# Performance work log

Measured on AMD Instinct MI355X. Metric: run time of the kernel, lower is better.

Reference implementation:

```python
import jax, jax.numpy as jnp
import numpy as np

EMB = 768
HEADS = 12
DH = EMB // HEADS


def setup_inputs() -> dict:
    key = jax.random.key(0)
    k = jax.random.split(key, 5)
    s = 0.02
    return {
        "x": jax.random.normal(k[0], (4, 2048, EMB), dtype=jnp.float32),
        "qkv_w": jax.random.normal(k[1], (3 * EMB, EMB), dtype=jnp.float32) * s,  # torch Linear weight [out,in]
        "qkv_b": jax.random.normal(k[2], (3 * EMB,), dtype=jnp.float32) * s,
        "proj_w": jax.random.normal(k[3], (EMB, EMB), dtype=jnp.float32) * s,
        "proj_b": jax.random.normal(k[4], (EMB,), dtype=jnp.float32) * s,
    }


def reference(x, qkv_w, qkv_b, proj_w, proj_b):
    b, n, _ = x.shape
    qkv = x @ qkv_w.T + qkv_b  # [b, n, 3*EMB]
    # rearrange 'b n (h d qkv) -> qkv b h n d'
    qkv = qkv.reshape(b, n, HEADS, DH, 3)
    qkv = jnp.transpose(qkv, (4, 0, 2, 1, 3))  # [3, b, h, n, d]
    q, k, v = qkv[0], qkv[1], qkv[2]
    e = jnp.einsum("bhqd,bhkd->bhqk", q, k)
    scale = jnp.float32(EMB) ** 0.5
    # NOTE: original divides by sqrt(emb_size) AFTER softmax (faithful to source)
    attn = jax.nn.softmax(e, axis=-1) / scale
    out = jnp.einsum("bhqk,bhkd->bhqd", attn, v)
    out = jnp.transpose(out, (0, 2, 1, 3)).reshape(b, n, EMB)  # 'b h n d -> b n (h d)'
    return out @ proj_w.T + proj_b
```

## Files before the change

kernel.cpp:

```cpp
#include <hip/hip_runtime.h>
#include <hip/hip_bf16.h>

typedef unsigned short ushort_t;
typedef __attribute__((ext_vector_type(8))) short s16x8;
typedef __attribute__((ext_vector_type(4))) float f32x4;
typedef __attribute__((ext_vector_type(16))) float f32x16;
typedef __attribute__((ext_vector_type(4))) unsigned int u32x4;

#define EMB 768
#define HEADS 12
#define DH 64
#define BATCH 4
#define SEQ 2048
#define MTOK (BATCH*SEQ)
#define NQKV (3*EMB)
#define LOG2E 1.44269504088896f

__device__ __forceinline__ ushort_t f2bf(float f) {
  unsigned u = __float_as_uint(f);
  u += 0x7fffu + ((u >> 16) & 1u);
  return (ushort_t)(u >> 16);
}
__device__ __forceinline__ unsigned pk2bf(float a, float b) {
  return (unsigned)f2bf(a) | ((unsigned)f2bf(b) << 16);
}
__device__ __forceinline__ unsigned cvtpk(float lo, float hi_) {
  unsigned d;
  asm("v_cvt_pk_bf16_f32 %0, %1, %2" : "=v"(d) : "v"(lo), "v"(hi_));
  return d;
}

__device__ __forceinline__ void gload_lds16(const void* g, void* l) {
  __builtin_amdgcn_global_load_lds(
      (const __attribute__((address_space(1))) unsigned*)g,
      (__attribute__((address_space(3))) unsigned*)l, 16, 0, 0);
}

__global__ void cvt_bf16(const float* __restrict__ in, ushort_t* __restrict__ out, int n4) {
  int i = blockIdx.x * blockDim.x + threadIdx.x;
  if (i >= n4) return;
  const float4 v = reinterpret_cast<const float4*>(in)[i];
  reinterpret_cast<uint2*>(out)[i] = make_uint2(pk2bf(v.x, v.y), pk2bf(v.z, v.w));
}

__global__ void cvt_wqkv(const float* __restrict__ w, const float* __restrict__ bias,
                         ushort_t* __restrict__ out, float* __restrict__ bias_p, int n4) {
  int i = blockIdx.x * blockDim.x + threadIdx.x;
  if (i >= n4) return;
  const int srcrow = i / 192;
  const int c4 = i - srcrow * 192;
  const int h = srcrow / 192;
  const int rem = srcrow - h * 192;
  const int d = rem / 3;
  const int which = rem - d * 3;
  const int dstrow = which * 768 + h * 64 + d;
  const float4 v = reinterpret_cast<const float4*>(w)[i];
  reinterpret_cast<uint2*>(out)[dstrow * 192 + c4] =
      make_uint2(pk2bf(v.x, v.y), pk2bf(v.z, v.w));
  if (c4 == 0) bias_p[dstrow] = bias[srcrow];
}

#define TM 128
#define TN 128
#define BKG 64

template<int MODE>
__global__ __launch_bounds__(256, 2) void gemm_bt(
    const ushort_t* __restrict__ A, const ushort_t* __restrict__ BT,
    const float* __restrict__ bias, float* __restrict__ Cf,
    ushort_t* __restrict__ Qd, ushort_t* __restrict__ Kd, ushort_t* __restrict__ Vt,
    int M, int N, int K)
{
  __shared__ alignas(16) ushort_t As[TM*BKG];
  __shared__ alignas(16) ushort_t Bs[TN*BKG];
  const int t = threadIdx.x;
  const int w = t >> 6, l = t & 63, g = l >> 4, r = l & 15;
  const int wr = w >> 1, wc = w & 1;
  int lin = blockIdx.y * gridDim.x + blockIdx.x;
  const int cpx = (gridDim.x * gridDim.y) >> 3;
  lin = (lin & 7) * cpx + (lin >> 3);
  const int m0 = (lin / gridDim.x) * TM, n0 = (lin - (lin / gridDim.x) * gridDim.x) * TN;

  f32x4 acc[4][4] = {};

  for (int kt = 0; kt < K; kt += BKG) {
#pragma unroll
    for (int p = 0; p < 4; ++p) {
      const int off = (t + p*256) * 16;
      const int row = off >> 7;
      const int scb = (off & 127) ^ ((row & 7) << 4);
      gload_lds16(A  + (size_t)(m0+row)*K + kt + (scb>>1), (char*)As + off);
      gload_lds16(BT + (size_t)(n0+row)*K + kt + (scb>>1), (char*)Bs + off);
    }
    __syncthreads();

    s16x8 fa[4][2], fb[4][2];
#pragma unroll
    for (int mi = 0; mi < 4; ++mi)
#pragma unroll
      for (int kk = 0; kk < 2; ++kk) {
        const int ra = wr*64 + mi*16 + r;
        fa[mi][kk] = *(const s16x8*)((const char*)As + ra*128 + ((g*16 + kk*64) ^ ((ra&7)<<4)));
        const int rb = wc*64 + mi*16 + r;
        fb[mi][kk] = *(const s16x8*)((const char*)Bs + rb*128 + ((g*16 + kk*64) ^ ((rb&7)<<4)));
      }
#pragma unroll
    for (int mi = 0; mi < 4; ++mi)
#pragma unroll
      for (int ni = 0; ni < 4; ++ni) {
        acc[mi][ni] = __builtin_amdgcn_mfma_f32_16x16x32_bf16(fa[mi][0], fb[ni][0], acc[mi][ni], 0,0,0);
        acc[mi][ni] = __builtin_amdgcn_mfma_f32_16x16x32_bf16(fa[mi][1], fb[ni][1], acc[mi][ni], 0,0,0);
      }
    __syncthreads();
  }

#pragma unroll
  for (int ni = 0; ni < 4; ++ni) {
    const int col = n0 + wc*64 + ni*16 + r;
    const float bv = bias[col];
    if (MODE == 0) {
#pragma unroll
      for (int mi = 0; mi < 4; ++mi)
#pragma unroll
        for (int q = 0; q < 4; ++q) {
          const int rowg = m0 + wr*64 + mi*16 + g*4 + q;
          Cf[(size_t)rowg * N + col] = acc[mi][ni][q] + bv;
        }
    } else {
      const int which = col / 768;
      const int h_ = (col - which * 768) >> 6;
      const int d_ = col & 63;
      if (which == 2) {
#pragma unroll
        for (int mi = 0; mi < 4; ++mi) {
          const int nn0 = m0 + wr*64 + mi*16 + g*4;
          const int bb = nn0 >> 11, nl = nn0 & 2047;
          const int np0 = (nl & ~12) | ((nl & 4) << 1) | ((nl & 8) >> 1);
          uint2 u;
          u.x = pk2bf(acc[mi][ni][0] + bv, acc[mi][ni][1] + bv);
          u.y = pk2bf(acc[mi][ni][2] + bv, acc[mi][ni][3] + bv);
          *reinterpret_cast<uint2*>(Vt + ((size_t)(bb*HEADS + h_)*DH + d_)*SEQ + np0) = u;
        }
      } else {
        ushort_t* dst = (which == 0) ? Qd : Kd;
        const float sc = (which == 0) ? LOG2E : 1.0f;
#pragma unroll
        for (int mi = 0; mi < 4; ++mi)
#pragma unroll
          for (int q = 0; q < 4; ++q) {
            const int rowg = m0 + wr*64 + mi*16 + g*4 + q;
            const int bb = rowg >> 11, nn = rowg & 2047;
            dst[((size_t)(bb*HEADS + h_)*SEQ + nn)*DH + d_] =
                f2bf((acc[mi][ni][q] + bv) * sc);
          }
      }
    }
  }
}

#define NTIL 32

__global__ __launch_bounds__(256, 3) void attn_fwd(
    const ushort_t* __restrict__ Qd, const ushort_t* __restrict__ Kd,
    const ushort_t* __restrict__ Vt, ushort_t* __restrict__ Oa)
{
  __shared__ alignas(16) char L[3][16384];
  char* Lc = &L[0][0];

  const int t = threadIdx.x;
  const int w = t >> 6, l = t & 63;
  const int c31 = l & 31, hi = l >> 5;
  const int blk = blockIdx.x;
  const int logical = (blk & 7) * 96 + (blk >> 3);
  const int bh = logical >> 4;
  const int qt = logical & 15;
  const int q0 = qt * 128 + w * 32;
  const int b = bh / HEADS, h = bh - b * HEADS;

  const ushort_t* Qp = Qd + (size_t)bh * SEQ * DH;
  const ushort_t* Kp = Kd + (size_t)bh * SEQ * DH;
  const ushort_t* Vp = Vt + (size_t)bh * DH * SEQ;

  s16x8 qf[4];
  {
    const ushort_t* qp = Qp + (size_t)(q0 + c31) * DH + hi * 8;
#pragma unroll
    for (int c = 0; c < 4; ++c) qf[c] = *(const s16x8*)(qp + c * 16);
  }

  f32x16 oacc0 = {}, oacc1 = {};
  float ps0 = 0.f, ps1 = 0.f, ps2 = 0.f, ps3 = 0.f;

  const int ldsb = hi * 1024 + c31 * 16;
  const ushort_t* ksrc0 = Kp + (size_t)l * DH + w * 16;
  const ushort_t* vsrc0 = Vp + (size_t)l * SEQ + w * 16;
  char* kdst0 = Lc + w * 2048 + l * 16;

#define STAGE(bufc, tile_)                                                         \
  {                                                                                \
    const int tl = (tile_);                                                        \
    const ushort_t* ks = ksrc0 + (size_t)tl * (64 * DH);                           \
    const ushort_t* vs = vsrc0 + tl * 64;                                          \
    char* kd = kdst0 + (bufc) * 16384;                                             \
    gload_lds16(ks,     kd);                                                       \
    gload_lds16(ks + 8, kd + 1024);                                                \
    gload_lds16(vs,     kd + 8192);                                                \
    gload_lds16(vs + 8, kd + 9216);                                                \
  }

#define KGROUP(bufc, kg)                                                           \
  {                                                                                \
    const char* base = Lc + (bufc) * 16384 + ldsb;                                 \
    s16x8 kf0 = *(const s16x8*)(base + ((kg)*512 + 0*2048));                       \
    s16x8 kf1 = *(const s16x8*)(base + ((kg)*512 + 1*2048));                       \
    s16x8 kf2 = *(const s16x8*)(base + ((kg)*512 + 2*2048));                       \
    s16x8 kf3 = *(const s16x8*)(base + ((kg)*512 + 3*2048));                       \
    s16x8 va00 = *(const s16x8*)(base + (8192 + (kg)*4096 + 0*2048 + 0*512));      \
    s16x8 va01 = *(const s16x8*)(base + (8192 + (kg)*4096 + 1*2048 + 0*512));      \
    s16x8 va10 = *(const s16x8*)(base + (8192 + (kg)*4096 + 0*2048 + 1*512));      \
    s16x8 va11 = *(const s16x8*)(base + (8192 + (kg)*4096 + 1*2048 + 1*512));      \
    __builtin_amdgcn_s_setprio(1);                                                 \
    f32x16 s = {};                                                                 \
    s = __builtin_amdgcn_mfma_f32_32x32x16_bf16(kf0, qf[0], s, 0, 0, 0);           \
    s = __builtin_amdgcn_mfma_f32_32x32x16_bf16(kf1, qf[1], s, 0, 0, 0);           \
    s = __builtin_amdgcn_mfma_f32_32x32x16_bf16(kf2, qf[2], s, 0, 0, 0);           \
    s = __builtin_amdgcn_mfma_f32_32x32x16_bf16(kf3, qf[3], s, 0, 0, 0);           \
    __builtin_amdgcn_s_setprio(0);                                                 \
    float pe[16];                                                                  \
    _Pragma("unroll")                                                              \
    for (int r2 = 0; r2 < 16; ++r2) pe[r2] = __builtin_amdgcn_exp2f(s[r2]);        \
    ps0 += (pe[0]  + pe[1])  + (pe[2]  + pe[3]);                                   \
    ps1 += (pe[4]  + pe[5])  + (pe[6]  + pe[7]);                                   \
    ps2 += (pe[8]  + pe[9])  + (pe[10] + pe[11]);                                  \
    ps3 += (pe[12] + pe[13]) + (pe[14] + pe[15]);                                  \
    u32x4 f0u = { cvtpk(pe[0],  pe[1]),  cvtpk(pe[2],  pe[3]),                     \
                  cvtpk(pe[4],  pe[5]),  cvtpk(pe[6],  pe[7]) };                   \
    u32x4 f1u = { cvtpk(pe[8],  pe[9]),  cvtpk(pe[10], pe[11]),                    \
                  cvtpk(pe[12], pe[13]), cvtpk(pe[14], pe[15]) };                  \
    const s16x8 pf0 = __builtin_bit_cast(s16x8, f0u);                              \
    const s16x8 pf1 = __builtin_bit_cast(s16x8, f1u);                              \
    __builtin_amdgcn_s_setprio(1);                                                 \
    oacc0 = __builtin_amdgcn_mfma_f32_32x32x16_bf16(va00, pf0, oacc0, 0, 0, 0);    \
    oacc0 = __builtin_amdgcn_mfma_f32_32x32x16_bf16(va01, pf1, oacc0, 0, 0, 0);    \
    oacc1 = __builtin_amdgcn_mfma_f32_32x32x16_bf16(va10, pf0, oacc1, 0, 0, 0);    \
    oacc1 = __builtin_amdgcn_mfma_f32_32x32x16_bf16(va11, pf1, oacc1, 0, 0, 0);    \
    __builtin_amdgcn_s_setprio(0);                                                 \
  }

#define ITER(bufcur, bufn2, tt)                                                    \
  {                                                                                \
    asm volatile("s_barrier" ::: "memory");                                        \
    const int nt2 = (tt) + 2 < NTIL ? (tt) + 2 : NTIL - 1;                         \
    STAGE(bufn2, nt2);                                                             \
    asm volatile("s_waitcnt vmcnt(8)" ::: "memory");                               \
    asm volatile("s_barrier" ::: "memory");                                        \
    KGROUP(bufcur, 0);                                                             \
    KGROUP(bufcur, 1);                                                             \
  }

  STAGE(0, 0);
  STAGE(1, 1);
  for (int tt = 0; tt < NTIL - 2; tt += 3) {
    ITER(0, 2, tt);
    ITER(1, 0, tt + 1);
    ITER(2, 1, tt + 2);
  }
  ITER(0, 2, 30);
  ITER(1, 0, 31);
#undef ITER
#undef KGROUP
#undef STAGE

  const float psum = (ps0 + ps1) + (ps2 + ps3);
  const float lt = psum + __shfl_xor(psum, 32);
  const float scale = 0.036084391824351615f / lt;

  ushort_t* op = Oa + ((size_t)(b * SEQ + q0 + c31)) * EMB + h * DH;
#pragma unroll
  for (int f = 0; f < 2; ++f) {
    const f32x16& o = f ? oacc1 : oacc0;
#pragma unroll
    for (int rq = 0; rq < 4; ++rq) {
      const int dbase = f * 32 + 8 * rq + 4 * hi;
      uint2 u;
      u.x = pk2bf(o[rq*4+0] * scale, o[rq*4+1] * scale);
      u.y = pk2bf(o[rq*4+2] * scale, o[rq*4+3] * scale);
      *reinterpret_cast<uint2*>(op + dbase) = u;
    }
  }
}

extern "C" void kernel_launch(void* const* d_in, const int* in_sizes, int n_in,
                              void* d_out, int out_size, void* d_ws, size_t ws_size,
                              hipStream_t stream) {
  const float* x      = (const float*)d_in[0];
  const float* qkv_w  = (const float*)d_in[1];
  const float* qkv_b  = (const float*)d_in[2];
  const float* proj_w = (const float*)d_in[3];
  const float* proj_b = (const float*)d_in[4];
  float* out = (float*)d_out;

  ushort_t* xb    = (ushort_t*)d_ws;
  ushort_t* wqkv  = xb    + (size_t)MTOK*EMB;
  ushort_t* wproj = wqkv  + (size_t)NQKV*EMB;
  ushort_t* Qd    = wproj + (size_t)EMB*EMB;
  ushort_t* Kd    = Qd    + (size_t)MTOK*EMB;
  ushort_t* Vt    = Kd    + (size_t)MTOK*EMB;
  ushort_t* Oa    = Vt    + (size_t)MTOK*EMB;
  float*    biasp = (float*)(Oa + (size_t)MTOK*EMB);

  {
    int n4 = MTOK*EMB/4;
    cvt_bf16<<<(n4+255)/256, 256, 0, stream>>>(x, xb, n4);
  }
  {
    int n4 = NQKV*EMB/4;
    cvt_wqkv<<<(n4+255)/256, 256, 0, stream>>>(qkv_w, qkv_b, wqkv, biasp, n4);
  }
  {
    int n4 = EMB*EMB/4;
    cvt_bf16<<<(n4+255)/256, 256, 0, stream>>>(proj_w, wproj, n4);
  }

  gemm_bt<1><<<dim3(NQKV/TN, MTOK/TM), 256, 0, stream>>>(
      xb, wqkv, biasp, nullptr, Qd, Kd, Vt, MTOK, NQKV, EMB);

  attn_fwd<<<768, 256, 0, stream>>>(Qd, Kd, Vt, Oa);

  gemm_bt<0><<<dim3(EMB/TN, MTOK/TM), 256, 0, stream>>>(
      Oa, wproj, proj_b, out, nullptr, nullptr, nullptr, MTOK, EMB, EMB);
}
```

Baseline: 145.8 us.

## Process 64 query rows per wave in attention to reuse K/V fragments

The attention kernel now runs 2 waves per block (128 threads), and each wave handles 64 query rows as two 32-row MFMA tiles. Every K and V fragment read from LDS is reused for both tiles, halving LDS reads per MFMA, and each wave issues twice as many global-to-LDS loads per stage, with the vmcnt wait adjusted to match. The cost is more accumulator and Q registers per wave (launch bounds lowered to 2) and fewer waves available to hide latency.

```diff
diff --git a/kernel.cpp b/kernel.cpp
--- a/kernel.cpp
+++ b/kernel.cpp
@@ -160,7 +160,7 @@
 
 #define NTIL 32
 
-__global__ __launch_bounds__(256, 3) void attn_fwd(
+__global__ __launch_bounds__(128, 2) void attn_fwd(
     const ushort_t* __restrict__ Qd, const ushort_t* __restrict__ Kd,
     const ushort_t* __restrict__ Vt, ushort_t* __restrict__ Oa)
 {
@@ -174,38 +174,41 @@
   const int logical = (blk & 7) * 96 + (blk >> 3);
   const int bh = logical >> 4;
   const int qt = logical & 15;
-  const int q0 = qt * 128 + w * 32;
+  const int q0 = qt * 128 + w * 64;
   const int b = bh / HEADS, h = bh - b * HEADS;
 
   const ushort_t* Qp = Qd + (size_t)bh * SEQ * DH;
   const ushort_t* Kp = Kd + (size_t)bh * SEQ * DH;
   const ushort_t* Vp = Vt + (size_t)bh * DH * SEQ;
 
-  s16x8 qf[4];
+  s16x8 qf0[4], qf1[4];
   {
-    const ushort_t* qp = Qp + (size_t)(q0 + c31) * DH + hi * 8;
-#pragma unroll
-    for (int c = 0; c < 4; ++c) qf[c] = *(const s16x8*)(qp + c * 16);
-  }
-
-  f32x16 oacc0 = {}, oacc1 = {};
-  float ps0 = 0.f, ps1 = 0.f, ps2 = 0.f, ps3 = 0.f;
+    const ushort_t* qp0 = Qp + (size_t)(q0 + c31) * DH + hi * 8;
+    const ushort_t* qp1 = qp0 + 32 * DH;
+#pragma unroll
+    for (int c = 0; c < 4; ++c) { qf0[c] = *(const s16x8*)(qp0 + c*16);
+                                  qf1[c] = *(const s16x8*)(qp1 + c*16); }
+  }
+
+  f32x16 oa00 = {}, oa01 = {};
+  f32x16 oa10 = {}, oa11 = {};
+  float ps00 = 0.f, ps01 = 0.f, ps10 = 0.f, ps11 = 0.f;
 
   const int ldsb = hi * 1024 + c31 * 16;
-  const ushort_t* ksrc0 = Kp + (size_t)l * DH + w * 16;
-  const ushort_t* vsrc0 = Vp + (size_t)l * SEQ + w * 16;
-  char* kdst0 = Lc + w * 2048 + l * 16;
+  const ushort_t* ksrc0 = Kp + (size_t)l * DH + w * 8;
+  const ushort_t* vsrc0 = Vp + (size_t)l * SEQ + w * 8;
+  char* kdst0 = Lc + w * 1024 + l * 16;
 
 #define STAGE(bufc, tile_)                                                         \
   {                                                                                \
-    const int tl = (tile_);                                                        \
-    const ushort_t* ks = ksrc0 + (size_t)tl * (64 * DH);                           \
-    const ushort_t* vs = vsrc0 + tl * 64;                                          \
+    const ushort_t* ks = ksrc0 + (size_t)(tile_) * (64 * DH);                      \
+    const ushort_t* vs = vsrc0 + (tile_) * 64;                                     \
     char* kd = kdst0 + (bufc) * 16384;                                             \
-    gload_lds16(ks,     kd);                                                       \
-    gload_lds16(ks + 8, kd + 1024);                                                \
-    gload_lds16(vs,     kd + 8192);                                                \
-    gload_lds16(vs + 8, kd + 9216);                                                \
+    _Pragma("unroll")                                                              \
+    for (int p = 0; p < 4; ++p) {                                                  \
+      gload_lds16(ks + p * 16, kd + p * 2048);                                     \
+      gload_lds16(vs + p * 16, kd + 8192 + p * 2048);                              \
+    }                                                                              \
   }
 
 #define KGROUP(bufc, kg)                                                           \
@@ -220,30 +223,47 @@
     s16x8 va10 = *(const s16x8*)(base + (8192 + (kg)*4096 + 0*2048 + 1*512));      \
     s16x8 va11 = *(const s16x8*)(base + (8192 + (kg)*4096 + 1*2048 + 1*512));      \
     __builtin_amdgcn_s_setprio(1);                                                 \
-    f32x16 s = {};                                                                 \
-    s = __builtin_amdgcn_mfma_f32_32x32x16_bf16(kf0, qf[0], s, 0, 0, 0);           \
-    s = __builtin_amdgcn_mfma_f32_32x32x16_bf16(kf1, qf[1], s, 0, 0, 0);           \
-    s = __builtin_amdgcn_mfma_f32_32x32x16_bf16(kf2, qf[2], s, 0, 0, 0);           \
-    s = __builtin_amdgcn_mfma_f32_32x32x16_bf16(kf3, qf[3], s, 0, 0, 0);           \
+    f32x16 s0 = {}, s1 = {};                                                       \
+    s0 = __builtin_amdgcn_mfma_f32_32x32x16_bf16(kf0, qf0[0], s0, 0, 0, 0);        \
+    s1 = __builtin_amdgcn_mfma_f32_32x32x16_bf16(kf0, qf1[0], s1, 0, 0, 0);        \
+    s0 = __builtin_amdgcn_mfma_f32_32x32x16_bf16(kf1, qf0[1], s0, 0, 0, 0);        \
+    s1 = __builtin_amdgcn_mfma_f32_32x32x16_bf16(kf1, qf1[1], s1, 0, 0, 0);        \
+    s0 = __builtin_amdgcn_mfma_f32_32x32x16_bf16(kf2, qf0[2], s0, 0, 0, 0);        \
+    s1 = __builtin_amdgcn_mfma_f32_32x32x16_bf16(kf2, qf1[2], s1, 0, 0, 0);        \
+    s0 = __builtin_amdgcn_mfma_f32_32x32x16_bf16(kf3, qf0[3], s0, 0, 0, 0);        \
+    s1 = __builtin_amdgcn_mfma_f32_32x32x16_bf16(kf3, qf1[3], s1, 0, 0, 0);        \
     __builtin_amdgcn_s_setprio(0);                                                 \
-    float pe[16];                                                                  \
+    float pe0[16], pe1[16];                                                        \
     _Pragma("unroll")                                                              \
-    for (int r2 = 0; r2 < 16; ++r2) pe[r2] = __builtin_amdgcn_exp2f(s[r2]);        \
-    ps0 += (pe[0]  + pe[1])  + (pe[2]  + pe[3]);                                   \
-    ps1 += (pe[4]  + pe[5])  + (pe[6]  + pe[7]);                                   \
-    ps2 += (pe[8]  + pe[9])  + (pe[10] + pe[11]);                                  \
-    ps3 += (pe[12] + pe[13]) + (pe[14] + pe[15]);                                  \
-    u32x4 f0u = { cvtpk(pe[0],  pe[1]),  cvtpk(pe[2],  pe[3]),                     \
-                  cvtpk(pe[4],  pe[5]),  cvtpk(pe[6],  pe[7]) };                   \
-    u32x4 f1u = { cvtpk(pe[8],  pe[9]),  cvtpk(pe[10], pe[11]),                    \
-                  cvtpk(pe[12], pe[13]), cvtpk(pe[14], pe[15]) };                  \
-    const s16x8 pf0 = __builtin_bit_cast(s16x8, f0u);                              \
-    const s16x8 pf1 = __builtin_bit_cast(s16x8, f1u);                              \
+    for (int r2 = 0; r2 < 16; ++r2) {                                              \
+      pe0[r2] = __builtin_amdgcn_exp2f(s0[r2]);                                    \
+      pe1[r2] = __builtin_amdgcn_exp2f(s1[r2]);                                    \
+    }                                                                              \
+    ps00 += ((pe0[0]+pe0[1])+(pe0[2]+pe0[3])) + ((pe0[4]+pe0[5])+(pe0[6]+pe0[7])); \
+    ps01 += ((pe0[8]+pe0[9])+(pe0[10]+pe0[11]))+((pe0[12]+pe0[13])+(pe0[14]+pe0[15]));\
+    ps10 += ((pe1[0]+pe1[1])+(pe1[2]+pe1[3])) + ((pe1[4]+pe1[5])+(pe1[6]+pe1[7])); \
+    ps11 += ((pe1[8]+pe1[9])+(pe1[10]+pe1[11]))+((pe1[12]+pe1[13])+(pe1[14]+pe1[15]));\
+    u32x4 a0 = { cvtpk(pe0[0],  pe0[1]),  cvtpk(pe0[2],  pe0[3]),                  \
+                 cvtpk(pe0[4],  pe0[5]),  cvtpk(pe0[6],  pe0[7]) };                \
+    u32x4 a1 = { cvtpk(pe0[8],  pe0[9]),  cvtpk(pe0[10], pe0[11]),                 \
+                 cvtpk(pe0[12], pe0[13]), cvtpk(pe0[14], pe0[15]) };               \
+    u32x4 b0 = { cvtpk(pe1[0],  pe1[1]),  cvtpk(pe1[2],  pe1[3]),                  \
+                 cvtpk(pe1[4],  pe1[5]),  cvtpk(pe1[6],  pe1[7]) };                \
+    u32x4 b1 = { cvtpk(pe1[8],  pe1[9]),  cvtpk(pe1[10], pe1[11]),                 \
+                 cvtpk(pe1[12], pe1[13]), cvtpk(pe1[14], pe1[15]) };               \
+    const s16x8 pf00 = __builtin_bit_cast(s16x8, a0);                              \
+    const s16x8 pf01 = __builtin_bit_cast(s16x8, a1);                              \
+    const s16x8 pf10 = __builtin_bit_cast(s16x8, b0);                              \
+    const s16x8 pf11 = __builtin_bit_cast(s16x8, b1);                              \
     __builtin_amdgcn_s_setprio(1);                                                 \
-    oacc0 = __builtin_amdgcn_mfma_f32_32x32x16_bf16(va00, pf0, oacc0, 0, 0, 0);    \
-    oacc0 = __builtin_amdgcn_mfma_f32_32x32x16_bf16(va01, pf1, oacc0, 0, 0, 0);    \
-    oacc1 = __builtin_amdgcn_mfma_f32_32x32x16_bf16(va10, pf0, oacc1, 0, 0, 0);    \
-    oacc1 = __builtin_amdgcn_mfma_f32_32x32x16_bf16(va11, pf1, oacc1, 0, 0, 0);    \
+    oa00 = __builtin_amdgcn_mfma_f32_32x32x16_bf16(va00, pf00, oa00, 0, 0, 0);     \
+    oa00 = __builtin_amdgcn_mfma_f32_32x32x16_bf16(va01, pf01, oa00, 0, 0, 0);     \
+    oa01 = __builtin_amdgcn_mfma_f32_32x32x16_bf16(va10, pf00, oa01, 0, 0, 0);     \
+    oa01 = __builtin_amdgcn_mfma_f32_32x32x16_bf16(va11, pf01, oa01, 0, 0, 0);     \
+    oa10 = __builtin_amdgcn_mfma_f32_32x32x16_bf16(va00, pf10, oa10, 0, 0, 0);     \
+    oa10 = __builtin_amdgcn_mfma_f32_32x32x16_bf16(va01, pf11, oa10, 0, 0, 0);     \
+    oa11 = __builtin_amdgcn_mfma_f32_32x32x16_bf16(va10, pf10, oa11, 0, 0, 0);     \
+    oa11 = __builtin_amdgcn_mfma_f32_32x32x16_bf16(va11, pf11, oa11, 0, 0, 0);     \
     __builtin_amdgcn_s_setprio(0);                                                 \
   }
 
@@ -252,7 +272,7 @@
     asm volatile("s_barrier" ::: "memory");                                        \
     const int nt2 = (tt) + 2 < NTIL ? (tt) + 2 : NTIL - 1;                         \
     STAGE(bufn2, nt2);                                                             \
-    asm volatile("s_waitcnt vmcnt(8)" ::: "memory");                               \
+    asm volatile("s_waitcnt vmcnt(16)" ::: "memory");                              \
     asm volatile("s_barrier" ::: "memory");                                        \
     KGROUP(bufcur, 0);                                                             \
     KGROUP(bufcur, 1);                                                             \
@@ -271,21 +291,28 @@
 #undef KGROUP
 #undef STAGE
 
-  const float psum = (ps0 + ps1) + (ps2 + ps3);
-  const float lt = psum + __shfl_xor(psum, 32);
-  const float scale = 0.036084391824351615f / lt;
-
-  ushort_t* op = Oa + ((size_t)(b * SEQ + q0 + c31)) * EMB + h * DH;
-#pragma unroll
-  for (int f = 0; f < 2; ++f) {
-    const f32x16& o = f ? oacc1 : oacc0;
-#pragma unroll
-    for (int rq = 0; rq < 4; ++rq) {
-      const int dbase = f * 32 + 8 * rq + 4 * hi;
-      uint2 u;
-      u.x = pk2bf(o[rq*4+0] * scale, o[rq*4+1] * scale);
-      u.y = pk2bf(o[rq*4+2] * scale, o[rq*4+3] * scale);
-      *reinterpret_cast<uint2*>(op + dbase) = u;
+  const float psum0 = ps00 + ps01;
+  const float psum1 = ps10 + ps11;
+  const float lt0 = psum0 + __shfl_xor(psum0, 32);
+  const float lt1 = psum1 + __shfl_xor(psum1, 32);
+  const float scale0 = 0.036084391824351615f / lt0;
+  const float scale1 = 0.036084391824351615f / lt1;
+
+#pragma unroll
+  for (int j = 0; j < 2; ++j) {
+    const float sc = j ? scale1 : scale0;
+    ushort_t* op = Oa + ((size_t)(b * SEQ + q0 + j*32 + c31)) * EMB + h * DH;
+#pragma unroll
+    for (int f = 0; f < 2; ++f) {
+      const f32x16& o = j ? (f ? oa11 : oa10) : (f ? oa01 : oa00);
+#pragma unroll
+      for (int rq = 0; rq < 4; ++rq) {
+        const int dbase = f * 32 + 8 * rq + 4 * hi;
+        uint2 u;
+        u.x = pk2bf(o[rq*4+0] * sc, o[rq*4+1] * sc);
+        u.y = pk2bf(o[rq*4+2] * sc, o[rq*4+3] * sc);
+        *reinterpret_cast<uint2*>(op + dbase) = u;
+      }
     }
   }
 }
@@ -325,7 +352,7 @@
   gemm_bt<1><<<dim3(NQKV/TN, MTOK/TM), 256, 0, stream>>>(
       xb, wqkv, biasp, nullptr, Qd, Kd, Vt, MTOK, NQKV, EMB);
 
-  attn_fwd<<<768, 256, 0, stream>>>(Qd, Kd, Vt, Oa);
+  attn_fwd<<<768, 128, 0, stream>>>(Qd, Kd, Vt, Oa);
 
   gemm_bt<0><<<dim3(EMB/TN, MTOK/TM), 256, 0, stream>>>(
       Oa, wproj, proj_b, out, nullptr, nullptr, nullptr, MTOK, EMB, EMB);
```

Measured after the change: 159.1 us. 1.09x slower.

## Use one barrier per K/V tile and batch both QK MFMA groups

Applied to the files above, without the earlier changes.

The attention main loop now prefetches only one tile ahead into a three-buffer ring, not two. This lets each iteration use a single barrier instead of two, and the wait becomes vmcnt(4). Each tile's eight K fragments are loaded together and both 32-key score blocks are computed back to back before the exp/PV phase, which gives the scheduler more independent MFMA work. The cost is a shorter prefetch distance, so global-load latency is less hidden, and register pressure is higher from holding two score accumulators at once.

```diff
diff --git a/kernel.cpp b/kernel.cpp
--- a/kernel.cpp
+++ b/kernel.cpp
@@ -208,27 +208,15 @@
     gload_lds16(vs + 8, kd + 9216);                                                \
   }
 
-#define KGROUP(bufc, kg)                                                           \
+#define SMPV(base, kg, sreg)                                                       \
   {                                                                                \
-    const char* base = Lc + (bufc) * 16384 + ldsb;                                 \
-    s16x8 kf0 = *(const s16x8*)(base + ((kg)*512 + 0*2048));                       \
-    s16x8 kf1 = *(const s16x8*)(base + ((kg)*512 + 1*2048));                       \
-    s16x8 kf2 = *(const s16x8*)(base + ((kg)*512 + 2*2048));                       \
-    s16x8 kf3 = *(const s16x8*)(base + ((kg)*512 + 3*2048));                       \
     s16x8 va00 = *(const s16x8*)(base + (8192 + (kg)*4096 + 0*2048 + 0*512));      \
     s16x8 va01 = *(const s16x8*)(base + (8192 + (kg)*4096 + 1*2048 + 0*512));      \
     s16x8 va10 = *(const s16x8*)(base + (8192 + (kg)*4096 + 0*2048 + 1*512));      \
     s16x8 va11 = *(const s16x8*)(base + (8192 + (kg)*4096 + 1*2048 + 1*512));      \
-    __builtin_amdgcn_s_setprio(1);                                                 \
-    f32x16 s = {};                                                                 \
-    s = __builtin_amdgcn_mfma_f32_32x32x16_bf16(kf0, qf[0], s, 0, 0, 0);           \
-    s = __builtin_amdgcn_mfma_f32_32x32x16_bf16(kf1, qf[1], s, 0, 0, 0);           \
-    s = __builtin_amdgcn_mfma_f32_32x32x16_bf16(kf2, qf[2], s, 0, 0, 0);           \
-    s = __builtin_amdgcn_mfma_f32_32x32x16_bf16(kf3, qf[3], s, 0, 0, 0);           \
-    __builtin_amdgcn_s_setprio(0);                                                 \
     float pe[16];                                                                  \
     _Pragma("unroll")                                                              \
-    for (int r2 = 0; r2 < 16; ++r2) pe[r2] = __builtin_amdgcn_exp2f(s[r2]);        \
+    for (int r2 = 0; r2 < 16; ++r2) pe[r2] = __builtin_amdgcn_exp2f(sreg[r2]);     \
     ps0 += (pe[0]  + pe[1])  + (pe[2]  + pe[3]);                                   \
     ps1 += (pe[4]  + pe[5])  + (pe[6]  + pe[7]);                                   \
     ps2 += (pe[8]  + pe[9])  + (pe[10] + pe[11]);                                  \
@@ -247,28 +235,52 @@
     __builtin_amdgcn_s_setprio(0);                                                 \
   }
 
-#define ITER(bufcur, bufn2, tt)                                                    \
+#define TILE(bufc)                                                                 \
   {                                                                                \
+    const char* base = Lc + (bufc) * 16384 + ldsb;                                 \
+    s16x8 kA0 = *(const s16x8*)(base + (0*512 + 0*2048));                          \
+    s16x8 kA1 = *(const s16x8*)(base + (0*512 + 1*2048));                          \
+    s16x8 kA2 = *(const s16x8*)(base + (0*512 + 2*2048));                          \
+    s16x8 kA3 = *(const s16x8*)(base + (0*512 + 3*2048));                          \
+    s16x8 kB0 = *(const s16x8*)(base + (1*512 + 0*2048));                          \
+    s16x8 kB1 = *(const s16x8*)(base + (1*512 + 1*2048));                          \
+    s16x8 kB2 = *(const s16x8*)(base + (1*512 + 2*2048));                          \
+    s16x8 kB3 = *(const s16x8*)(base + (1*512 + 3*2048));                          \
+    f32x16 sA = {}, sB = {};                                                       \
+    __builtin_amdgcn_s_setprio(1);                                                 \
+    sA = __builtin_amdgcn_mfma_f32_32x32x16_bf16(kA0, qf[0], sA, 0, 0, 0);         \
+    sA = __builtin_amdgcn_mfma_f32_32x32x16_bf16(kA1, qf[1], sA, 0, 0, 0);         \
+    sA = __builtin_amdgcn_mfma_f32_32x32x16_bf16(kA2, qf[2], sA, 0, 0, 0);         \
+    sA = __builtin_amdgcn_mfma_f32_32x32x16_bf16(kA3, qf[3], sA, 0, 0, 0);         \
+    sB = __builtin_amdgcn_mfma_f32_32x32x16_bf16(kB0, qf[0], sB, 0, 0, 0);         \
+    sB = __builtin_amdgcn_mfma_f32_32x32x16_bf16(kB1, qf[1], sB, 0, 0, 0);         \
+    sB = __builtin_amdgcn_mfma_f32_32x32x16_bf16(kB2, qf[2], sB, 0, 0, 0);         \
+    sB = __builtin_amdgcn_mfma_f32_32x32x16_bf16(kB3, qf[3], sB, 0, 0, 0);         \
+    __builtin_amdgcn_s_setprio(0);                                                 \
+    SMPV(base, 0, sA);                                                             \
+    SMPV(base, 1, sB);                                                             \
+  }
+
+#define ITER(bufcur, bufnxt, tt)                                                   \
+  {                                                                                \
+    const int ntl = (tt) + 1 < NTIL ? (tt) + 1 : NTIL - 1;                         \
+    STAGE(bufnxt, ntl);                                                            \
+    asm volatile("s_waitcnt vmcnt(4)" ::: "memory");                               \
     asm volatile("s_barrier" ::: "memory");                                        \
-    const int nt2 = (tt) + 2 < NTIL ? (tt) + 2 : NTIL - 1;                         \
-    STAGE(bufn2, nt2);                                                             \
-    asm volatile("s_waitcnt vmcnt(8)" ::: "memory");                               \
-    asm volatile("s_barrier" ::: "memory");                                        \
-    KGROUP(bufcur, 0);                                                             \
-    KGROUP(bufcur, 1);                                                             \
+    TILE(bufcur);                                                                  \
   }
 
   STAGE(0, 0);
-  STAGE(1, 1);
   for (int tt = 0; tt < NTIL - 2; tt += 3) {
-    ITER(0, 2, tt);
-    ITER(1, 0, tt + 1);
-    ITER(2, 1, tt + 2);
-  }
-  ITER(0, 2, 30);
-  ITER(1, 0, 31);
+    ITER(0, 1, tt);
+    ITER(1, 2, tt + 1);
+    ITER(2, 0, tt + 2);
+  }
+  ITER(0, 1, 30);
+  ITER(1, 2, 31);
 #undef ITER
-#undef KGROUP
+#undef TILE
+#undef SMPV
 #undef STAGE
 
   const float psum = (ps0 + ps1) + (ps2 + ps3);
```

Result: slower. 149.5 us (+2.5%).

## Triple-buffer GEMM K loop with async LDS prefetch two stages ahead

Applied to the files above, without the earlier changes.

Replaces the single-buffered 64-wide K loop with a three-stage LDS ring of 32-wide K slices. Global-to-LDS loads are issued two stages ahead and waited on with vmcnt, so memory latency overlaps with MFMA work. MFMA sections run at raised wave priority, and launch bounds ask for three blocks per CU. The loop hardcodes 24 steps, which ties it to K=768. The unswizzled 64-byte LDS rows may cause bank conflicts.

```diff
diff --git a/kernel.cpp b/kernel.cpp
--- a/kernel.cpp
+++ b/kernel.cpp
@@ -62,17 +62,17 @@
 
 #define TM 128
 #define TN 128
-#define BKG 64
+#define NSTEP 24
 
 template<int MODE>
-__global__ __launch_bounds__(256, 2) void gemm_bt(
+__global__ __launch_bounds__(256, 3) void gemm_bt(
     const ushort_t* __restrict__ A, const ushort_t* __restrict__ BT,
     const float* __restrict__ bias, float* __restrict__ Cf,
     ushort_t* __restrict__ Qd, ushort_t* __restrict__ Kd, ushort_t* __restrict__ Vt,
     int M, int N, int K)
 {
-  __shared__ alignas(16) ushort_t As[TM*BKG];
-  __shared__ alignas(16) ushort_t Bs[TN*BKG];
+  __shared__ alignas(16) ushort_t As[3][TM*32];
+  __shared__ alignas(16) ushort_t Bs[3][TN*32];
   const int t = threadIdx.x;
   const int w = t >> 6, l = t & 63, g = l >> 4, r = l & 15;
   const int wr = w >> 1, wc = w & 1;
@@ -83,36 +83,62 @@
 
   f32x4 acc[4][4] = {};
 
-  for (int kt = 0; kt < K; kt += BKG) {
-#pragma unroll
-    for (int p = 0; p < 4; ++p) {
-      const int off = (t + p*256) * 16;
-      const int row = off >> 7;
-      const int scb = (off & 127) ^ ((row & 7) << 4);
-      gload_lds16(A  + (size_t)(m0+row)*K + kt + (scb>>1), (char*)As + off);
-      gload_lds16(BT + (size_t)(n0+row)*K + kt + (scb>>1), (char*)Bs + off);
-    }
-    __syncthreads();
-
-    s16x8 fa[4][2], fb[4][2];
-#pragma unroll
-    for (int mi = 0; mi < 4; ++mi)
-#pragma unroll
-      for (int kk = 0; kk < 2; ++kk) {
-        const int ra = wr*64 + mi*16 + r;
-        fa[mi][kk] = *(const s16x8*)((const char*)As + ra*128 + ((g*16 + kk*64) ^ ((ra&7)<<4)));
-        const int rb = wc*64 + mi*16 + r;
-        fb[mi][kk] = *(const s16x8*)((const char*)Bs + rb*128 + ((g*16 + kk*64) ^ ((rb&7)<<4)));
-      }
-#pragma unroll
-    for (int mi = 0; mi < 4; ++mi)
-#pragma unroll
-      for (int ni = 0; ni < 4; ++ni) {
-        acc[mi][ni] = __builtin_amdgcn_mfma_f32_16x16x32_bf16(fa[mi][0], fb[ni][0], acc[mi][ni], 0,0,0);
-        acc[mi][ni] = __builtin_amdgcn_mfma_f32_16x16x32_bf16(fa[mi][1], fb[ni][1], acc[mi][ni], 0,0,0);
-      }
-    __syncthreads();
-  }
+#define GSTAGE(bufc, st)                                                           \
+  {                                                                                \
+    const int kt = (st) * 32;                                                      \
+    _Pragma("unroll")                                                              \
+    for (int p = 0; p < 2; ++p) {                                                  \
+      const int i = t + p * 256;                              \
+      const int row = i >> 2, c8 = (i & 3) * 8;                                    \
+      gload_lds16(A  + (size_t)(m0 + row) * K + kt + c8,                           \
+                  (char*)&As[bufc][0] + i * 16);                                   \
+      gload_lds16(BT + (size_t)(n0 + row) * K + kt + c8,                           \
+                  (char*)&Bs[bufc][0] + i * 16);                                   \
+    }                                                                              \
+  }
+
+#define GCOMP(bufc)                                                                \
+  {                                                                                \
+    const char* ab = (const char*)&As[bufc][0] + wr * 4096 + r * 64 + g * 16;      \
+    const char* bb = (const char*)&Bs[bufc][0] + wc * 4096 + r * 64 + g * 16;      \
+    s16x8 fa[4], fb[4];                                                            \
+    _Pragma("unroll")                                                              \
+    for (int mi = 0; mi < 4; ++mi) {                                               \
+      fa[mi] = *(const s16x8*)(ab + mi * 1024);                                    \
+      fb[mi] = *(const s16x8*)(bb + mi * 1024);                                    \
+    }                                                                              \
+    __builtin_amdgcn_s_setprio(1);                                                 \
+    _Pragma("unroll")                                                              \
+    for (int mi = 0; mi < 4; ++mi)                                                 \
+      _Pragma("unroll")                                                            \
+      for (int ni = 0; ni < 4; ++ni)                                               \
+        acc[mi][ni] = __builtin_amdgcn_mfma_f32_16x16x32_bf16(                     \
+            fa[mi], fb[ni], acc[mi][ni], 0, 0, 0);                                 \
+    __builtin_amdgcn_s_setprio(0);                                                 \
+  }
+
+#define GITER(bufcur, bufn2, st)                                                   \
+  {                                                                                \
+    asm volatile("s_barrier" ::: "memory");                                        \
+    { const int s2 = (st) + 2 < NSTEP ? (st) + 2 : NSTEP - 1; GSTAGE(bufn2, s2); } \
+    asm volatile("s_waitcnt vmcnt(8)" ::: "memory");                               \
+    asm volatile("s_barrier" ::: "memory");                                        \
+    GCOMP(bufcur);                                                                 \
+  }
+
+  GSTAGE(0, 0);
+  GSTAGE(1, 1);
+  for (int s = 0; s < NSTEP - 3; s += 3) {
+    GITER(0, 2, s);
+    GITER(1, 0, s + 1);
+    GITER(2, 1, s + 2);
+  }
+  GITER(0, 2, 21);
+  GITER(1, 0, 22);
+  GITER(2, 1, 23);
+#undef GITER
+#undef GCOMP
+#undef GSTAGE
 
 #pragma unroll
   for (int ni = 0; ni < 4; ++ni) {
```

After: 154.0 us. +5.6%, slower.
